# Optimization experiments

Measured on AMD Instinct MI355X. Metric: run time of the kernel, lower is better.

## Reference

```python
import jax, jax.numpy as jnp
import numpy as np

EPS = 1e-5  # torch LayerNorm default

def setup_inputs() -> dict:
    key = jax.random.key(0)
    ks = jax.random.split(key, 4)
    B, S, D, R = 4, 4096, 2048, 64
    x = jax.random.normal(ks[0], (B, S, D), dtype=jnp.float32)
    # LayerNorm params (torch init: gamma=1, beta=0)
    ln_gamma = jnp.ones((D,), dtype=jnp.float32)
    ln_beta = jnp.zeros((D,), dtype=jnp.float32)
    # down_proj: kaiming_uniform_(a=sqrt(5)) -> U(-bound, bound), bound = sqrt(6/((1+5)*fan_in)) = 1/sqrt(fan_in)
    bound = 1.0 / np.sqrt(D)
    w_down = jax.random.uniform(ks[1], (R, D), minval=-bound, maxval=bound, dtype=jnp.float32)
    b_down = jnp.zeros((R,), dtype=jnp.float32)
    # up_proj is zero-initialized in the original; use small random values so the output is non-trivial
    w_up = jax.random.normal(ks[2], (D, R), dtype=jnp.float32) * 0.02
    b_up = jnp.zeros((D,), dtype=jnp.float32)
    scale = jnp.ones((1,), dtype=jnp.float32)  # learnable_scalar init
    return {"x": x, "ln_gamma": ln_gamma, "ln_beta": ln_beta,
            "w_down": w_down, "b_down": b_down,
            "w_up": w_up, "b_up": b_up, "scale": scale}


def reference(x, ln_gamma, ln_beta, w_down, b_down, w_up, b_up, scale):
    # adapter_layernorm_option == 'in': LN before down-projection
    mu = jnp.mean(x, axis=-1, keepdims=True)
    var = jnp.mean(jnp.square(x - mu), axis=-1, keepdims=True)
    h = (x - mu) * jax.lax.rsqrt(var + EPS) * ln_gamma + ln_beta
    # down-proj + ReLU (dropout is identity in eval / p=0)
    down = jax.nn.relu(jnp.einsum('bsd,rd->bsr', h, w_down) + b_down)
    # up-proj, scale, residual
    up = (jnp.einsum('bsr,dr->bsd', down, w_up) + b_up) * scale
    return up + x
```

## Files before the change

kernel.cpp:

```cpp
#include <hip/hip_runtime.h>

#define D 2048
#define R 64
#define NTOK 16384
#define KT 256
#define KW 512
#define HROW 264
#define PROW 68
#define WREG 8448

typedef float f32x4 __attribute__((ext_vector_type(4)));
typedef short s16x8 __attribute__((ext_vector_type(8)));

__device__ inline unsigned short f2bf(float f) {
    union { float f; unsigned int u; } c; c.f = f;
    unsigned int u = c.u;
    return (unsigned short)((u + 0x7fffu + ((u >> 16) & 1u)) >> 16);
}

__global__ __launch_bounds__(256)
void convert_w(const float* __restrict__ wd, const float* __restrict__ wu,
               unsigned short* __restrict__ wdb, unsigned short* __restrict__ wub) {
    const int i = blockIdx.x * 256 + threadIdx.x;
    const float4 a = ((const float4*)wd)[i];
    const float4 b = ((const float4*)wu)[i];
    ushort4 pa, pb;
    pa.x = f2bf(a.x); pa.y = f2bf(a.y); pa.z = f2bf(a.z); pa.w = f2bf(a.w);
    pb.x = f2bf(b.x); pb.y = f2bf(b.y); pb.z = f2bf(b.z); pb.w = f2bf(b.w);
    ((ushort4*)wdb)[i] = pa;
    ((ushort4*)wub)[i] = pb;
}

__global__ __launch_bounds__(256)
void prep_uc(const float* __restrict__ wd, const float* __restrict__ gamma,
             const float* __restrict__ beta, const float* __restrict__ bd,
             float* __restrict__ u, float* __restrict__ cb) {
    const int r = blockIdx.x;
    const int tid = threadIdx.x;
    const int lane = tid & 63, wave = tid >> 6;
    float su = 0.f, sc = 0.f;
    for (int i = tid; i < D / 4; i += 256) {
        const float4 w  = ((const float4*)(wd + (size_t)r * D))[i];
        const float4 g  = ((const float4*)gamma)[i];
        const float4 be = ((const float4*)beta)[i];
        su += w.x * g.x + w.y * g.y + w.z * g.z + w.w * g.w;
        sc += w.x * be.x + w.y * be.y + w.z * be.z + w.w * be.w;
    }
    #pragma unroll
    for (int off = 32; off >= 1; off >>= 1) {
        su += __shfl_xor(su, off, 64);
        sc += __shfl_xor(sc, off, 64);
    }
    __shared__ float red[2][4];
    if (lane == 0) { red[0][wave] = su; red[1][wave] = sc; }
    __syncthreads();
    if (tid == 0) {
        u[r]  = red[0][0] + red[0][1] + red[0][2] + red[0][3];
        cb[r] = red[1][0] + red[1][1] + red[1][2] + red[1][3] + bd[r];
    }
}

__global__ __launch_bounds__(256, 4)
void adapter_mfma(const float* __restrict__ x,
                  const float* __restrict__ gamma,
                  const unsigned short* __restrict__ wdb,
                  const unsigned short* __restrict__ wub,
                  const float* __restrict__ u,
                  const float* __restrict__ cb,
                  const float* __restrict__ bu,
                  const float* __restrict__ scale_p,
                  float* __restrict__ out)
{
    __shared__ __align__(16) unsigned char smem[4][WREG];
    __shared__ float s_lds[4][16];
    __shared__ float ss_lds[4][16];

    const int tid  = threadIdx.x;
    const int wave = tid >> 6;
    const int lane = tid & 63;
    const int l15  = lane & 15;
    const int quad = lane >> 4;
    const int tok0 = blockIdx.x * 16;

    unsigned short* h = (unsigned short*)smem[wave];
    float*          pw = (float*)smem[wave];

    float sm[16], ssm[16];
    #pragma unroll
    for (int m = 0; m < 16; ++m) { sm[m] = 0.f; ssm[m] = 0.f; }

    f32x4 acc[4];
    #pragma unroll
    for (int nt = 0; nt < 4; ++nt) acc[nt] = (f32x4){0.f, 0.f, 0.f, 0.f};

    const int kbase = wave * KW;
    #pragma unroll
    for (int kt = 0; kt < KW / KT; ++kt) {
        const int kb = kbase + kt * KT;
        const float4 g4 = ((const float4*)gamma)[(kb >> 2) + lane];
        #pragma unroll
        for (int m = 0; m < 16; ++m) {
            const float4 v = ((const float4*)(x + (size_t)(tok0 + m) * D + kb))[lane];
            sm[m]  += (v.x + v.y) + (v.z + v.w);
            ssm[m] += (v.x * v.x + v.y * v.y) + (v.z * v.z + v.w * v.w);
            ushort4 hp;
            hp.x = f2bf(v.x * g4.x);
            hp.y = f2bf(v.y * g4.y);
            hp.z = f2bf(v.z * g4.z);
            hp.w = f2bf(v.w * g4.w);
            *(ushort4*)&h[m * HROW + lane * 4] = hp;
        }
        #pragma unroll
        for (int s = 0; s < KT / 32; ++s) {
            const s16x8 a = *(const s16x8*)&h[l15 * HROW + s * 32 + quad * 8];
            const int kg = kb + s * 32 + quad * 8;
            #pragma unroll
            for (int nt = 0; nt < 4; ++nt) {
                const s16x8 b = *(const s16x8*)&wdb[(size_t)(nt * 16 + l15) * D + kg];
                acc[nt] = __builtin_amdgcn_mfma_f32_16x16x32_bf16(a, b, acc[nt], 0, 0, 0);
            }
        }
    }

    #pragma unroll
    for (int m = 0; m < 16; ++m) {
        float s = sm[m], q = ssm[m];
        #pragma unroll
        for (int off = 32; off >= 1; off >>= 1) {
            s += __shfl_xor(s, off, 64);
            q += __shfl_xor(q, off, 64);
        }
        sm[m] = s; ssm[m] = q;
    }
    if (lane == 0) {
        #pragma unroll
        for (int m = 0; m < 16; ++m) { s_lds[wave][m] = sm[m]; ss_lds[wave][m] = ssm[m]; }
    }

    #pragma unroll
    for (int nt = 0; nt < 4; ++nt)
        #pragma unroll
        for (int reg = 0; reg < 4; ++reg)
            pw[(quad * 4 + reg) * PROW + nt * 16 + l15] = acc[nt][reg];

    __syncthreads();

    const float s_tot  = s_lds[0][l15] + s_lds[1][l15] + s_lds[2][l15] + s_lds[3][l15];
    const float ss_tot = ss_lds[0][l15] + ss_lds[1][l15] + ss_lds[2][l15] + ss_lds[3][l15];
    const float mu = s_tot * (1.0f / D);
    const float rs = rsqrtf(ss_tot * (1.0f / D) - mu * mu + 1e-5f);

    s16x8 afrag[2];
    #pragma unroll
    for (int f = 0; f < 2; ++f) {
        const int rb = f * 32 + quad * 8;
        float ps[8];
        #pragma unroll
        for (int e = 0; e < 8; ++e) ps[e] = 0.f;
        #pragma unroll
        for (int w = 0; w < 4; ++w) {
            const float* pv = (const float*)smem[w];
            const f32x4 pA = *(const f32x4*)&pv[l15 * PROW + rb];
            const f32x4 pB = *(const f32x4*)&pv[l15 * PROW + rb + 4];
            ps[0] += pA[0]; ps[1] += pA[1]; ps[2] += pA[2]; ps[3] += pA[3];
            ps[4] += pB[0]; ps[5] += pB[1]; ps[6] += pB[2]; ps[7] += pB[3];
        }
        const f32x4 u0 = *(const f32x4*)&u[rb];
        const f32x4 u1 = *(const f32x4*)&u[rb + 4];
        const f32x4 c0 = *(const f32x4*)&cb[rb];
        const f32x4 c1 = *(const f32x4*)&cb[rb + 4];
        s16x8 af;
        #pragma unroll
        for (int e = 0; e < 4; ++e) {
            const float v0 = fmaxf(rs * (ps[e]     - mu * u0[e]) + c0[e], 0.f);
            const float v1 = fmaxf(rs * (ps[4 + e] - mu * u1[e]) + c1[e], 0.f);
            af[e]     = (short)f2bf(v0);
            af[4 + e] = (short)f2bf(v1);
        }
        afrag[f] = af;
    }

    const float scl = scale_p[0];
    const int nbase = wave * 512;
    #pragma unroll 4
    for (int t = 0; t < 32; ++t) {
        const int dd = nbase + t * 16 + l15;
        const s16x8 b0 = *(const s16x8*)&wub[(size_t)dd * R + quad * 8];
        const s16x8 b1 = *(const s16x8*)&wub[(size_t)dd * R + 32 + quad * 8];
        f32x4 c = (f32x4){0.f, 0.f, 0.f, 0.f};
        c = __builtin_amdgcn_mfma_f32_16x16x32_bf16(afrag[0], b0, c, 0, 0, 0);
        c = __builtin_amdgcn_mfma_f32_16x16x32_bf16(afrag[1], b1, c, 0, 0, 0);
        const float bun = bu[dd];
        #pragma unroll
        for (int reg = 0; reg < 4; ++reg) {
            const int m = quad * 4 + reg;
            const size_t idx = (size_t)(tok0 + m) * D + dd;
            out[idx] = scl * (c[reg] + bun) + x[idx];
        }
    }
}

extern "C" void kernel_launch(void* const* d_in, const int* in_sizes, int n_in,
                              void* d_out, int out_size, void* d_ws, size_t ws_size,
                              hipStream_t stream) {
    const float* x     = (const float*)d_in[0];
    const float* gamma = (const float*)d_in[1];
    const float* beta  = (const float*)d_in[2];
    const float* wd    = (const float*)d_in[3];
    const float* bd    = (const float*)d_in[4];
    const float* wu    = (const float*)d_in[5];
    const float* bu    = (const float*)d_in[6];
    const float* scl   = (const float*)d_in[7];
    float* out = (float*)d_out;

    unsigned short* wdb = (unsigned short*)d_ws;
    unsigned short* wub = wdb + (size_t)R * D;
    float* u  = (float*)(wub + (size_t)D * R);
    float* cb = u + R;

    convert_w<<<(R * D / 4) / 256, 256, 0, stream>>>(wd, wu, wdb, wub);
    prep_uc<<<R, 256, 0, stream>>>(wd, gamma, beta, bd, u, cb);
    adapter_mfma<<<NTOK / 16, 256, 0, stream>>>(x, gamma, wdb, wub, u, cb, bu, scl, out);
}
```

Measured before the change: 358.9 us.

## Pre-pack bf16 weights in MFMA fragment order and stage epilogue through LDS

The weight-conversion kernel now writes both bf16 weight matrices in MFMA fragment order, so each lane's B-operand load becomes one contiguous 16-byte read per fragment instead of a strided gather. The up-projection epilogue writes MFMA results to an LDS staging buffer and then emits coalesced float4 reads of x and float4 nontemporal stores of out. This replaces the earlier scattered scalar accesses. The cost is an extra block barrier and LDS traffic, plus reuse of the per-wave LDS region.

```diff
diff --git a/kernel.cpp b/kernel.cpp
--- a/kernel.cpp
+++ b/kernel.cpp
@@ -7,6 +7,7 @@
 #define KW 512
 #define HROW 264
 #define PROW 68
+#define SROW 132
 #define WREG 8448
 
 typedef float f32x4 __attribute__((ext_vector_type(4)));
@@ -17,18 +18,39 @@
     unsigned int u = c.u;
     return (unsigned short)((u + 0x7fffu + ((u >> 16) & 1u)) >> 16);
 }
+__device__ inline ushort4 pack4(float4 v) {
+    ushort4 p;
+    p.x = f2bf(v.x); p.y = f2bf(v.y); p.z = f2bf(v.z); p.w = f2bf(v.w);
+    return p;
+}
 
 __global__ __launch_bounds__(256)
-void convert_w(const float* __restrict__ wd, const float* __restrict__ wu,
-               unsigned short* __restrict__ wdb, unsigned short* __restrict__ wub) {
-    const int i = blockIdx.x * 256 + threadIdx.x;
-    const float4 a = ((const float4*)wd)[i];
-    const float4 b = ((const float4*)wu)[i];
-    ushort4 pa, pb;
-    pa.x = f2bf(a.x); pa.y = f2bf(a.y); pa.z = f2bf(a.z); pa.w = f2bf(a.w);
-    pb.x = f2bf(b.x); pb.y = f2bf(b.y); pb.z = f2bf(b.z); pb.w = f2bf(b.w);
-    ((ushort4*)wdb)[i] = pa;
-    ((ushort4*)wub)[i] = pb;
+void convert_pack(const float* __restrict__ wd, const float* __restrict__ wu,
+                  unsigned short* __restrict__ wdbp, unsigned short* __restrict__ wubp) {
+    const int fid  = blockIdx.x * 256 + threadIdx.x;
+    const int lane = fid & 63;
+    const int l15  = lane & 15;
+    const int quad = lane >> 4;
+    {
+        const int nt = (fid >> 6) & 3;
+        const int ks = fid >> 8;
+        const int r  = nt * 16 + l15;
+        const int k0 = ks * 32 + quad * 8;
+        const float4 a0 = *(const float4*)(wd + (size_t)r * D + k0);
+        const float4 a1 = *(const float4*)(wd + (size_t)r * D + k0 + 4);
+        *(ushort4*)(wdbp + (size_t)fid * 8)     = pack4(a0);
+        *(ushort4*)(wdbp + (size_t)fid * 8 + 4) = pack4(a1);
+    }
+    {
+        const int s   = (fid >> 6) & 1;
+        const int nt2 = fid >> 7;
+        const int dd  = nt2 * 16 + l15;
+        const int r0  = s * 32 + quad * 8;
+        const float4 b0 = *(const float4*)(wu + (size_t)dd * R + r0);
+        const float4 b1 = *(const float4*)(wu + (size_t)dd * R + r0 + 4);
+        *(ushort4*)(wubp + (size_t)fid * 8)     = pack4(b0);
+        *(ushort4*)(wubp + (size_t)fid * 8 + 4) = pack4(b1);
+    }
 }
 
 __global__ __launch_bounds__(256)
@@ -63,8 +85,8 @@
 __global__ __launch_bounds__(256, 4)
 void adapter_mfma(const float* __restrict__ x,
                   const float* __restrict__ gamma,
-                  const unsigned short* __restrict__ wdb,
-                  const unsigned short* __restrict__ wub,
+                  const unsigned short* __restrict__ wdbp,
+                  const unsigned short* __restrict__ wubp,
                   const float* __restrict__ u,
                   const float* __restrict__ cb,
                   const float* __restrict__ bu,
@@ -82,7 +104,7 @@
     const int quad = lane >> 4;
     const int tok0 = blockIdx.x * 16;
 
-    unsigned short* h = (unsigned short*)smem[wave];
+    unsigned short* h  = (unsigned short*)smem[wave];
     float*          pw = (float*)smem[wave];
 
     float sm[16], ssm[16];
@@ -103,20 +125,17 @@
             const float4 v = ((const float4*)(x + (size_t)(tok0 + m) * D + kb))[lane];
             sm[m]  += (v.x + v.y) + (v.z + v.w);
             ssm[m] += (v.x * v.x + v.y * v.y) + (v.z * v.z + v.w * v.w);
-            ushort4 hp;
-            hp.x = f2bf(v.x * g4.x);
-            hp.y = f2bf(v.y * g4.y);
-            hp.z = f2bf(v.z * g4.z);
-            hp.w = f2bf(v.w * g4.w);
-            *(ushort4*)&h[m * HROW + lane * 4] = hp;
-        }
+            float4 hg;
+            hg.x = v.x * g4.x; hg.y = v.y * g4.y; hg.z = v.z * g4.z; hg.w = v.w * g4.w;
+            *(ushort4*)&h[m * HROW + lane * 4] = pack4(hg);
+        }
+        const int ks0 = (kb >> 5);
         #pragma unroll
         for (int s = 0; s < KT / 32; ++s) {
             const s16x8 a = *(const s16x8*)&h[l15 * HROW + s * 32 + quad * 8];
-            const int kg = kb + s * 32 + quad * 8;
             #pragma unroll
             for (int nt = 0; nt < 4; ++nt) {
-                const s16x8 b = *(const s16x8*)&wdb[(size_t)(nt * 16 + l15) * D + kg];
+                const s16x8 b = ((const s16x8*)wdbp)[((ks0 + s) * 4 + nt) * 64 + lane];
                 acc[nt] = __builtin_amdgcn_mfma_f32_16x16x32_bf16(a, b, acc[nt], 0, 0, 0);
             }
         }
@@ -180,22 +199,44 @@
         afrag[f] = af;
     }
 
+    __syncthreads();
+
     const float scl = scale_p[0];
+    float* stg = (float*)smem[wave];
     const int nbase = wave * 512;
-    #pragma unroll 4
-    for (int t = 0; t < 32; ++t) {
-        const int dd = nbase + t * 16 + l15;
-        const s16x8 b0 = *(const s16x8*)&wub[(size_t)dd * R + quad * 8];
-        const s16x8 b1 = *(const s16x8*)&wub[(size_t)dd * R + 32 + quad * 8];
-        f32x4 c = (f32x4){0.f, 0.f, 0.f, 0.f};
-        c = __builtin_amdgcn_mfma_f32_16x16x32_bf16(afrag[0], b0, c, 0, 0, 0);
-        c = __builtin_amdgcn_mfma_f32_16x16x32_bf16(afrag[1], b1, c, 0, 0, 0);
-        const float bun = bu[dd];
-        #pragma unroll
-        for (int reg = 0; reg < 4; ++reg) {
-            const int m = quad * 4 + reg;
-            const size_t idx = (size_t)(tok0 + m) * D + dd;
-            out[idx] = scl * (c[reg] + bun) + x[idx];
+    #pragma unroll
+    for (int c = 0; c < 4; ++c) {
+        const int dbase = nbase + c * 128;
+        const int nt2_0 = dbase >> 4;
+        #pragma unroll
+        for (int t = 0; t < 8; ++t) {
+            const s16x8 b0 = ((const s16x8*)wubp)[((nt2_0 + t) * 2 + 0) * 64 + lane];
+            const s16x8 b1 = ((const s16x8*)wubp)[((nt2_0 + t) * 2 + 1) * 64 + lane];
+            f32x4 cc = (f32x4){0.f, 0.f, 0.f, 0.f};
+            cc = __builtin_amdgcn_mfma_f32_16x16x32_bf16(afrag[0], b0, cc, 0, 0, 0);
+            cc = __builtin_amdgcn_mfma_f32_16x16x32_bf16(afrag[1], b1, cc, 0, 0, 0);
+            #pragma unroll
+            for (int reg = 0; reg < 4; ++reg)
+                stg[(quad * 4 + reg) * SROW + t * 16 + l15] = cc[reg];
+        }
+        #pragma unroll
+        for (int j = 0; j < 2; ++j) {
+            const int dloc = j * 64 + l15 * 4;
+            const int dd   = dbase + dloc;
+            const float4 bu4 = *(const float4*)(bu + dd);
+            #pragma unroll
+            for (int mg = 0; mg < 4; ++mg) {
+                const int m = mg * 4 + quad;
+                const f32x4 v = *(const f32x4*)&stg[m * SROW + dloc];
+                const size_t idx = (size_t)(tok0 + m) * D + dd;
+                const float4 xv = *(const float4*)(x + idx);
+                f32x4 o;
+                o[0] = scl * (v[0] + bu4.x) + xv.x;
+                o[1] = scl * (v[1] + bu4.y) + xv.y;
+                o[2] = scl * (v[2] + bu4.z) + xv.z;
+                o[3] = scl * (v[3] + bu4.w) + xv.w;
+                __builtin_nontemporal_store(o, (f32x4*)(out + idx));
+            }
         }
     }
 }
@@ -213,12 +254,12 @@
     const float* scl   = (const float*)d_in[7];
     float* out = (float*)d_out;
 
-    unsigned short* wdb = (unsigned short*)d_ws;
-    unsigned short* wub = wdb + (size_t)R * D;
-    float* u  = (float*)(wub + (size_t)D * R);
+    unsigned short* wdbp = (unsigned short*)d_ws;
+    unsigned short* wubp = wdbp + (size_t)R * D;
+    float* u  = (float*)(wubp + (size_t)D * R);
     float* cb = u + R;
 
-    convert_w<<<(R * D / 4) / 256, 256, 0, stream>>>(wd, wu, wdb, wub);
+    convert_pack<<<(R * D / 8) / 256, 256, 0, stream>>>(wd, wu, wdbp, wubp);
     prep_uc<<<R, 256, 0, stream>>>(wd, gamma, beta, bd, u, cb);
-    adapter_mfma<<<NTOK / 16, 256, 0, stream>>>(x, gamma, wdb, wub, u, cb, bu, scl, out);
-}
+    adapter_mfma<<<NTOK / 16, 256, 0, stream>>>(x, gamma, wdbp, wubp, u, cb, bu, scl, out);
+}
```

Measured after the change: 323.9 us. -9.7%, faster.
